# Kernel optimization log

Measured on AMD Instinct MI355X. Metric: run time of the kernel, lower is better.

The kernel has to match this reference:

```python
import jax, jax.numpy as jnp
import numpy as np

B, T, C, H = 16, 2048, 1024, 128  # BATCH_SIZE, BLOCK_SIZE, EMBEDDING_SIZE, HEAD_SIZE


def setup_inputs() -> dict:
    key = jax.random.key(0)
    kx, kk, kq, kv = jax.random.split(key, 4)
    x = jax.random.normal(kx, (B, T, C), dtype=jnp.float32)
    # torch Linear(C, H, bias=False): y = x @ W^T with W [H, C]; we store W^T as [C, H]
    scale = C ** -0.5
    Wk = jax.random.normal(kk, (C, H), dtype=jnp.float32) * scale
    Wq = jax.random.normal(kq, (C, H), dtype=jnp.float32) * scale
    Wv = jax.random.normal(kv, (C, H), dtype=jnp.float32) * scale
    return {"x": x, "Wk": Wk, "Wq": Wq, "Wv": Wv}


def reference(x, Wk, Wq, Wv):
    # projections: [B, T, H]
    k = jnp.einsum("btc,ch->bth", x, Wk)
    q = jnp.einsum("btc,ch->bth", x, Wq)
    v = jnp.einsum("btc,ch->bth", x, Wv)
    # scaled scores: [B, T, T]
    scores = jnp.einsum("bqh,bkh->bqk", q, k) * (H ** -0.5)
    # causal mask (tril) then softmax over keys
    causal = jnp.tril(jnp.ones((T, T), dtype=bool))
    scores = jnp.where(causal, scores, -jnp.inf)
    weights = jax.nn.softmax(scores, axis=-1)
    # dropout with p=0.0 is identity (eval mode)
    return jnp.einsum("bqk,bkh->bqh", weights, v)
```

## Files before the change

kernel.cpp:

```cpp
#include <hip/hip_runtime.h>
#include <cmath>

#define B_ 16
#define T_ 2048
#define C_ 1024
#define H_ 128

#define BQ 64
#define BK 64
#define PS 68

#define PM 64
#define PK 64

typedef __bf16 bf16;
typedef bf16 bf16x8 __attribute__((ext_vector_type(8)));
typedef bf16 bf16x4 __attribute__((ext_vector_type(4)));
typedef float f32x4 __attribute__((ext_vector_type(4)));

#define GL_LDS16(gptr, lptr)                                                     \
    __builtin_amdgcn_global_load_lds(                                            \
        (const __attribute__((address_space(1))) unsigned int*)(gptr),           \
        (__attribute__((address_space(3))) unsigned int*)(lptr), 16, 0, 0)

__global__ __launch_bounds__(256) void convert_w(
    const float* __restrict__ Wq, const float* __restrict__ Wk,
    const float* __restrict__ Wv, bf16* __restrict__ wt)
{
    int gid = blockIdx.x * 256 + threadIdx.x;
    int w   = gid >> 14;
    int rem = gid & 16383;
    int n   = rem >> 7;
    int k0  = (rem & 127) * 8;
    const float* src = (w == 0) ? Wq : (w == 1) ? Wk : Wv;
    bf16x8 o;
#pragma unroll
    for (int j = 0; j < 8; ++j) o[j] = (bf16)src[(size_t)(k0 + j) * H_ + n];
    *(bf16x8*)(wt + (size_t)w * (H_ * C_) + (size_t)n * C_ + k0) = o;
}

__global__ __launch_bounds__(256, 2) void proj_mfma(
    const float* __restrict__ x, const bf16* __restrict__ wt,
    bf16* __restrict__ qb, bf16* __restrict__ kb, bf16* __restrict__ vtp)
{
    __shared__ bf16 xs[PM * PK];
    __shared__ bf16 ws[3 * H_ * PK];

    const int tid  = threadIdx.x;
    const int wave = tid >> 6;
    const int lane = tid & 63;
    const int quad = lane >> 4;
    const int lq   = lane & 15;
    const int wr   = wave >> 1;
    const int wc   = wave & 1;
    const int m0   = blockIdx.x * PM;
    const int phase = (blockIdx.x >> 3) & 15;

    f32x4 acc[3][2][4];
#pragma unroll
    for (int w = 0; w < 3; ++w)
#pragma unroll
        for (int mt = 0; mt < 2; ++mt)
#pragma unroll
            for (int nt = 0; nt < 4; ++nt)
                acc[w][mt][nt] = (f32x4){0.f, 0.f, 0.f, 0.f};

    int woff[12];
#pragma unroll
    for (int j = 0; j < 12; ++j) {
        int s  = (wave * 12 + j) * 64 + lane;
        int w  = s >> 10;
        int n  = (s >> 3) & 127;
        int cs = s & 7;
        int c  = cs ^ (n & 7);
        woff[j] = w * (H_ * C_) + n * C_ + c * 8;
    }
    int xoff[4], xslot[4];
#pragma unroll
    for (int j = 0; j < 4; ++j) {
        int f4  = j * 256 + tid;
        int row = f4 >> 4;
        int c4  = f4 & 15;
        int c   = c4 >> 1, half = c4 & 1;
        xoff[j]  = (m0 + row) * C_ + c4 * 4;
        xslot[j] = (row * 8 + (c ^ (row & 7))) * 8 + half * 4;
    }

    float4 xv[4];
#pragma unroll
    for (int j = 0; j < 4; ++j)
        xv[j] = *(const float4*)(x + (size_t)xoff[j] + phase * PK);

    const int NT = C_ / PK;
    for (int t = 0; t < NT; ++t) {
        const int k0 = (((t + phase) & 15)) * PK;
        __syncthreads();
#pragma unroll
        for (int j = 0; j < 12; ++j) {
            GL_LDS16(wt + woff[j] + k0, (char*)ws + (wave * 12 + j) * 1024);
        }
#pragma unroll
        for (int j = 0; j < 4; ++j) {
            bf16x4 o = {(bf16)xv[j].x, (bf16)xv[j].y, (bf16)xv[j].z, (bf16)xv[j].w};
            *(bf16x4*)&xs[xslot[j]] = o;
        }
        __syncthreads();

        if (t + 1 < NT) {
            const int k1 = (((t + 1 + phase) & 15)) * PK;
#pragma unroll
            for (int j = 0; j < 4; ++j)
                xv[j] = *(const float4*)(x + (size_t)xoff[j] + k1);
        }

#pragma unroll
        for (int kc = 0; kc < 2; ++kc) {
            const int c = kc * 4 + quad;
            bf16x8 af[2];
#pragma unroll
            for (int mt = 0; mt < 2; ++mt) {
                int row  = wr * 32 + mt * 16 + lq;
                int slot = row * 8 + (c ^ (row & 7));
                af[mt] = *(const bf16x8*)&xs[slot * 8];
            }
#pragma unroll
            for (int w = 0; w < 3; ++w) {
#pragma unroll
                for (int nt = 0; nt < 4; ++nt) {
                    int n    = wc * 64 + nt * 16 + lq;
                    int slot = n * 8 + (c ^ (n & 7));
                    bf16x8 bfr = *(const bf16x8*)&ws[w * (H_ * PK) + slot * 8];
                    acc[w][0][nt] = __builtin_amdgcn_mfma_f32_16x16x32_bf16(af[0], bfr, acc[w][0][nt], 0, 0, 0);
                    acc[w][1][nt] = __builtin_amdgcn_mfma_f32_16x16x32_bf16(af[1], bfr, acc[w][1][nt], 0, 0, 0);
                }
            }
        }
    }

    const int b  = m0 >> 11;
    const int t0 = m0 & (T_ - 1);
#pragma unroll
    for (int w = 0; w < 2; ++w) {
        bf16* dst = (w == 0) ? qb : kb;
#pragma unroll
        for (int mt = 0; mt < 2; ++mt)
#pragma unroll
            for (int nt = 0; nt < 4; ++nt)
#pragma unroll
                for (int r = 0; r < 4; ++r) {
                    int row = m0 + wr * 32 + mt * 16 + quad * 4 + r;
                    int h   = wc * 64 + nt * 16 + lq;
                    dst[(size_t)row * H_ + h] = (bf16)acc[w][mt][nt][r];
                }
    }
#pragma unroll
    for (int mt = 0; mt < 2; ++mt)
#pragma unroll
        for (int nt = 0; nt < 4; ++nt) {
            int h = wc * 64 + nt * 16 + lq;
            int t = t0 + wr * 32 + mt * 16 + quad * 4;
            bf16x4 o = {(bf16)acc[2][mt][nt][0], (bf16)acc[2][mt][nt][1],
                        (bf16)acc[2][mt][nt][2], (bf16)acc[2][mt][nt][3]};
            *(bf16x4*)&vtp[((size_t)b * H_ + h) * T_ + t] = o;
        }
}

__global__ __launch_bounds__(256) void attn_mfma(
    const bf16* __restrict__ qb, const bf16* __restrict__ kb,
    const bf16* __restrict__ vt, float* __restrict__ out)
{
    __shared__ bf16 Ks[2][BK * 128];
    __shared__ bf16 Vs[2][128 * BK];
    __shared__ bf16 Ps[4][16 * PS];

    const int tid  = threadIdx.x;
    const int wave = tid >> 6;
    const int lane = tid & 63;
    const int quad = lane >> 4;
    const int lq   = lane & 15;

    const int bid = blockIdx.x;
    const int b   = bid & 15;
    const int jq  = bid >> 4;
    const int t0b = (31 - jq) * BQ;
    const int qt0 = t0b + wave * 16;

    const bf16* qrow = qb + ((size_t)b * T_ + qt0 + lq) * H_ + quad * 8;
    bf16x8 qf[4];
#pragma unroll
    for (int c = 0; c < 4; ++c) qf[c] = *(const bf16x8*)(qrow + 32 * c);

    f32x4 acc[8];
#pragma unroll
    for (int i = 0; i < 8; ++i) acc[i] = (f32x4){0.f, 0.f, 0.f, 0.f};
    f32x4 l_acc = (f32x4){0.f, 0.f, 0.f, 0.f};

    bf16x8 ones;
#pragma unroll
    for (int j = 0; j < 8; ++j) ones[j] = (bf16)1.0f;

    const float SC2 = 0.12751749985029928f;
    const int ntiles = t0b / BK + 1;

    const bf16* Kg = kb + (size_t)b * T_ * H_;
    const bf16* Vg = vt + (size_t)b * H_ * T_;
    bf16* Pw = &Ps[wave][0];

    int koff[4], voff[4], dst8[4];
#pragma unroll
    for (int j = 0; j < 4; ++j) {
        int p   = (j * 4 + wave) * 64 + lane;
        int r   = p >> 4, pos = p & 15;
        int l   = (pos & 8) | ((pos & 7) ^ (r & 7));
        koff[j] = r * H_ + l * 8;
        int hh  = p >> 3, pos2 = p & 7;
        voff[j] = hh * T_ + (pos2 ^ (hh & 7)) * 8;
        dst8[j] = (j * 4 + wave) * 64 * 8;
    }
    int swk[4], swv[2];
#pragma unroll
    for (int c = 0; c < 4; ++c) {
        int l = quad + 4 * c;
        swk[c] = (l & 8) | ((l & 7) ^ (lq & 7));
    }
#pragma unroll
    for (int kc = 0; kc < 2; ++kc) swv[kc] = (quad + 4 * kc) ^ (lq & 7);

#pragma unroll
    for (int j = 0; j < 4; ++j) {
        GL_LDS16(Kg + (size_t)koff[j], &Ks[0][dst8[j]]);
        GL_LDS16(Vg + (size_t)voff[j], &Vs[0][dst8[j]]);
    }

    for (int kt = 0; kt < ntiles; ++kt) {
        __syncthreads();
        if (kt + 1 < ntiles) {
            const int k1 = (kt + 1) * BK;
            const int nb = (kt + 1) & 1;
#pragma unroll
            for (int j = 0; j < 4; ++j) {
                GL_LDS16(Kg + (size_t)k1 * H_ + koff[j], &Ks[nb][dst8[j]]);
                GL_LDS16(Vg + (size_t)(k1 + voff[j]),    &Vs[nb][dst8[j]]);
            }
        }
        const bf16* Kb = &Ks[kt & 1][0];
        const bf16* Vb = &Vs[kt & 1][0];
        const bool finalt = (kt == ntiles - 1);

#pragma unroll
        for (int ns = 0; ns < 4; ++ns) {
            if (!finalt || ns <= wave) {
                f32x4 sv = (f32x4){0.f, 0.f, 0.f, 0.f};
#pragma unroll
                for (int c = 0; c < 4; ++c) {
                    bf16x8 kf = *(const bf16x8*)&Kb[((ns * 16 + lq) * 16 + swk[c]) * 8];
                    sv = __builtin_amdgcn_mfma_f32_16x16x32_bf16(qf[c], kf, sv, 0, 0, 0);
                }
                if (finalt && ns == wave) {
#pragma unroll
                    for (int r = 0; r < 4; ++r) {
                        float p = (lq <= quad * 4 + r) ? exp2f(sv[r] * SC2) : 0.f;
                        Pw[(quad * 4 + r) * PS + ns * 16 + lq] = (bf16)p;
                    }
                } else {
#pragma unroll
                    for (int r = 0; r < 4; ++r) {
                        Pw[(quad * 4 + r) * PS + ns * 16 + lq] = (bf16)exp2f(sv[r] * SC2);
                    }
                }
            } else {
#pragma unroll
                for (int r = 0; r < 4; ++r)
                    Pw[(quad * 4 + r) * PS + ns * 16 + lq] = (bf16)0.f;
            }
        }

        bf16x8 pf[2];
#pragma unroll
        for (int kc = 0; kc < 2; ++kc)
            pf[kc] = *(const bf16x8*)&Pw[lq * PS + kc * 32 + quad * 8];

        l_acc = __builtin_amdgcn_mfma_f32_16x16x32_bf16(pf[0], ones, l_acc, 0, 0, 0);
        l_acc = __builtin_amdgcn_mfma_f32_16x16x32_bf16(pf[1], ones, l_acc, 0, 0, 0);

#pragma unroll
        for (int ht = 0; ht < 8; ++ht) {
#pragma unroll
            for (int kc = 0; kc < 2; ++kc) {
                bf16x8 vf = *(const bf16x8*)&Vb[((ht * 16 + lq) * 8 + swv[kc]) * 8];
                acc[ht] = __builtin_amdgcn_mfma_f32_16x16x32_bf16(pf[kc], vf, acc[ht], 0, 0, 0);
            }
        }
    }

    float inv[4];
#pragma unroll
    for (int r = 0; r < 4; ++r) inv[r] = 1.f / l_acc[r];
#pragma unroll
    for (int ht = 0; ht < 8; ++ht) {
#pragma unroll
        for (int r = 0; r < 4; ++r) {
            out[((size_t)b * T_ + qt0 + quad * 4 + r) * H_ + ht * 16 + lq] = acc[ht][r] * inv[r];
        }
    }
}

extern "C" void kernel_launch(void* const* d_in, const int* in_sizes, int n_in,
                              void* d_out, int out_size, void* d_ws, size_t ws_size,
                              hipStream_t stream) {
    const float* x  = (const float*)d_in[0];
    const float* Wk = (const float*)d_in[1];
    const float* Wq = (const float*)d_in[2];
    const float* Wv = (const float*)d_in[3];
    float* out = (float*)d_out;

    bf16* qb = (bf16*)d_ws;
    bf16* kb = qb + (size_t)B_ * T_ * H_;
    bf16* vt = kb + (size_t)B_ * T_ * H_;
    bf16* wt = vt + (size_t)B_ * T_ * H_;

    convert_w<<<192, 256, 0, stream>>>(Wq, Wk, Wv, wt);

    proj_mfma<<<(B_ * T_) / PM, 256, 0, stream>>>(x, wt, qb, kb, vt);

    attn_mfma<<<(T_ / BQ) * B_, 256, 0, stream>>>(qb, kb, vt, out);
}
```

Baseline: 278.3 us.

## Load K and V tiles directly from global memory instead of LDS staging

Drops the double-buffered LDS staging of K and V tiles, which used async global-to-LDS loads. Each wave now reads its K and V MFMA fragments straight from global memory. This removes LDS capacity pressure and the swizzled LDS reads, but each wave loads the same K/V data separately. It also loses the prefetch overlap, so more global and L2 traffic and exposed load latency are likely.

```diff
diff --git a/kernel.cpp b/kernel.cpp
--- a/kernel.cpp
+++ b/kernel.cpp
@@ -169,8 +169,6 @@
     const bf16* __restrict__ qb, const bf16* __restrict__ kb,
     const bf16* __restrict__ vt, float* __restrict__ out)
 {
-    __shared__ bf16 Ks[2][BK * 128];
-    __shared__ bf16 Vs[2][128 * BK];
     __shared__ bf16 Ps[4][16 * PS];
 
     const int tid  = threadIdx.x;
@@ -206,54 +204,19 @@
     const bf16* Vg = vt + (size_t)b * H_ * T_;
     bf16* Pw = &Ps[wave][0];
 
-    int koff[4], voff[4], dst8[4];
-#pragma unroll
-    for (int j = 0; j < 4; ++j) {
-        int p   = (j * 4 + wave) * 64 + lane;
-        int r   = p >> 4, pos = p & 15;
-        int l   = (pos & 8) | ((pos & 7) ^ (r & 7));
-        koff[j] = r * H_ + l * 8;
-        int hh  = p >> 3, pos2 = p & 7;
-        voff[j] = hh * T_ + (pos2 ^ (hh & 7)) * 8;
-        dst8[j] = (j * 4 + wave) * 64 * 8;
-    }
-    int swk[4], swv[2];
-#pragma unroll
-    for (int c = 0; c < 4; ++c) {
-        int l = quad + 4 * c;
-        swk[c] = (l & 8) | ((l & 7) ^ (lq & 7));
-    }
-#pragma unroll
-    for (int kc = 0; kc < 2; ++kc) swv[kc] = (quad + 4 * kc) ^ (lq & 7);
-
-#pragma unroll
-    for (int j = 0; j < 4; ++j) {
-        GL_LDS16(Kg + (size_t)koff[j], &Ks[0][dst8[j]]);
-        GL_LDS16(Vg + (size_t)voff[j], &Vs[0][dst8[j]]);
-    }
-
     for (int kt = 0; kt < ntiles; ++kt) {
         __syncthreads();
-        if (kt + 1 < ntiles) {
-            const int k1 = (kt + 1) * BK;
-            const int nb = (kt + 1) & 1;
-#pragma unroll
-            for (int j = 0; j < 4; ++j) {
-                GL_LDS16(Kg + (size_t)k1 * H_ + koff[j], &Ks[nb][dst8[j]]);
-                GL_LDS16(Vg + (size_t)(k1 + voff[j]),    &Vs[nb][dst8[j]]);
-            }
-        }
-        const bf16* Kb = &Ks[kt & 1][0];
-        const bf16* Vb = &Vs[kt & 1][0];
+        const int kbase = kt * BK;
         const bool finalt = (kt == ntiles - 1);
 
 #pragma unroll
         for (int ns = 0; ns < 4; ++ns) {
             if (!finalt || ns <= wave) {
+                const bf16* krow = Kg + (size_t)(kbase + ns * 16 + lq) * H_ + quad * 8;
                 f32x4 sv = (f32x4){0.f, 0.f, 0.f, 0.f};
 #pragma unroll
                 for (int c = 0; c < 4; ++c) {
-                    bf16x8 kf = *(const bf16x8*)&Kb[((ns * 16 + lq) * 16 + swk[c]) * 8];
+                    bf16x8 kf = *(const bf16x8*)(krow + 32 * c);
                     sv = __builtin_amdgcn_mfma_f32_16x16x32_bf16(qf[c], kf, sv, 0, 0, 0);
                 }
                 if (finalt && ns == wave) {
@@ -285,9 +248,10 @@
 
 #pragma unroll
         for (int ht = 0; ht < 8; ++ht) {
+            const bf16* vrow = Vg + (size_t)(ht * 16 + lq) * T_ + kbase + quad * 8;
 #pragma unroll
             for (int kc = 0; kc < 2; ++kc) {
-                bf16x8 vf = *(const bf16x8*)&Vb[((ht * 16 + lq) * 8 + swv[kc]) * 8];
+                bf16x8 vf = *(const bf16x8*)(vrow + 32 * kc);
                 acc[ht] = __builtin_amdgcn_mfma_f32_16x16x32_bf16(pf[kc], vf, acc[ht], 0, 0, 0);
             }
         }
```

After: 409.1 us. +47.0%, slower.
